# Kernel tuning notes

Hardware: AMD Instinct MI355X
Metric: run time of the kernel (lower is better)

## Reference

```python
import jax, jax.numpy as jnp
import numpy as np

B, C, H, W = 8, 64, 64, 64
OUT_H, OUT_W = 32, 32


def setup_inputs() -> dict:
    key = jax.random.key(0)
    ks = jax.random.split(key, 9)
    s = 1.0 / np.sqrt(C).astype(np.float32)
    return {
        "x": jax.random.normal(ks[0], (B, C, H, W), jnp.float32),
        "wq": jax.random.normal(ks[1], (C, C), jnp.float32) * s,
        "bq": jax.random.normal(ks[2], (C,), jnp.float32) * 0.01,
        "wk": jax.random.normal(ks[3], (C, C), jnp.float32) * s,
        "bk": jax.random.normal(ks[4], (C,), jnp.float32) * 0.01,
        "wv": jax.random.normal(ks[5], (C, C), jnp.float32) * s,
        "bv": jax.random.normal(ks[6], (C,), jnp.float32) * 0.01,
        "wm": jax.random.normal(ks[7], (C, C), jnp.float32) * s,
        "bm": jax.random.normal(ks[8], (C,), jnp.float32) * 0.01,
    }


def reference(x, wq, bq, wk, bk, wv, bv, wm, bm):
    # pushforward: self-attention over spatial tokens, 1x1-conv mixing + ReLU,
    # then bilinear resize to out_shape (align_corners=False semantics).
    b, c, h, w = x.shape
    t = x.reshape(b, c, h * w).transpose(0, 2, 1)  # [B, HW, C] tokens
    q = jnp.einsum('bnc,dc->bnd', t, wq) + bq      # 1x1 conv == per-pixel linear
    k = jnp.einsum('bnc,dc->bnd', t, wk) + bk
    v = jnp.einsum('bnc,dc->bnd', t, wv) + bv
    scores = jnp.einsum('bnc,bmc->bnm', q, k) / jnp.sqrt(jnp.float32(c))  # [B, HW, HW]
    attn = jax.nn.softmax(scores, axis=-1)
    o = jnp.einsum('bnm,bmc->bnc', attn, v)        # [B, HW, C]
    mixed = jax.nn.relu(jnp.einsum('bnc,dc->bnd', o, wm) + bm)
    out = mixed.transpose(0, 2, 1).reshape(b, c, h, w)
    # F.interpolate(mode='bilinear', align_corners=False) == half-pixel bilinear, no antialias
    out = jax.image.resize(out, (b, c, OUT_H, OUT_W), method='bilinear', antialias=False)
    return out
```

## Files before the change

### kernel.cpp

```cpp
#include <hip/hip_runtime.h>
#include <stdint.h>

typedef unsigned short u16;
typedef unsigned int   u32;
typedef __attribute__((ext_vector_type(8))) short short8;
typedef __attribute__((ext_vector_type(4))) float f32x4;

#define NTOK 4096
#define LOG2E 1.44269504088896340736f
#define QS    (0.125f * LOG2E)

__device__ __forceinline__ u16 f2bf(float f) {
    u32 u = __builtin_bit_cast(u32, f);
    u += 0x7fffu + ((u >> 16) & 1u);
    return (u16)(u >> 16);
}
__device__ __forceinline__ float bf2f(u16 v) {
    return __builtin_bit_cast(float, (u32)v << 16);
}
__device__ __forceinline__ u32 pk_hu(float a, float b) {
    u32 ua = __builtin_bit_cast(u32, a) + 0x8000u;
    u32 ub = __builtin_bit_cast(u32, b) + 0x8000u;
    return __builtin_amdgcn_perm(ub, ua, 0x07060302);
}

#define MFMA16x32 __builtin_amdgcn_mfma_f32_16x16x32_bf16

__global__ __launch_bounds__(256) void qkv_mfma4(
    const float* __restrict__ x,
    const float* __restrict__ wq, const float* __restrict__ bq,
    const float* __restrict__ wk, const float* __restrict__ bk,
    const float* __restrict__ wv, const float* __restrict__ bv,
    u16* __restrict__ Q, u16* __restrict__ K, u16* __restrict__ Vp)
{
    __shared__ __align__(16) u16 Wl[3 * 64 * 72];
    __shared__ __align__(16) u16 Xl[64 * 64];
    const int tid  = threadIdx.x;
    const int b    = blockIdx.x & 7;
    const int slab = blockIdx.x >> 3;
    const int n0   = slab << 6;
    const int wave = tid >> 6;
    const int lane = tid & 63;
    const int quad = lane >> 4;
    const int l15  = lane & 15;

#pragma unroll
    for (int j = 0; j < 12; ++j) {
        const float* src = (j < 4) ? wq : (j < 8) ? wk : wv;
        const float sc = (j < 4) ? QS : 1.0f;
        const int idx = (j & 3) * 1024 + tid * 4;
        const float4 v = *(const float4*)(src + idx);
        uint2 pk;
        pk.x = (u32)f2bf(v.x * sc) | ((u32)f2bf(v.y * sc) << 16);
        pk.y = (u32)f2bf(v.z * sc) | ((u32)f2bf(v.w * sc) << 16);
        *(uint2*)&Wl[(j >> 2) * 4608 + (idx >> 6) * 72 + (idx & 63)] = pk;
    }

    float4 xs[4];
#pragma unroll
    for (int g = 0; g < 4; ++g) {
        const int ch = g * 16 + wave * 4 + quad;
        xs[g] = *(const float4*)(x + ((size_t)(b * 64 + ch)) * NTOK + n0 + l15 * 4);
    }
#pragma unroll
    for (int g = 0; g < 4; ++g) {
        const int ch = g * 16 + wave * 4 + quad;
        const float vv[4] = {xs[g].x, xs[g].y, xs[g].z, xs[g].w};
#pragma unroll
        for (int e = 0; e < 4; ++e) {
            const int tok = l15 * 4 + e;
            Xl[tok * 64 + (((ch >> 3) ^ (tok & 7)) & 7) * 8 + (ch & 7)] = f2bf(vv[e]);
        }
    }
    __syncthreads();

    const int row0 = wave * 16 + l15;
    short8 xf[2];
#pragma unroll
    for (int kk = 0; kk < 2; ++kk)
        xf[kk] = *(const short8*)&Xl[row0 * 64 + (((kk * 4 + quad) ^ (row0 & 7)) & 7) * 8];

    const size_t tokbase = (size_t)b * NTOK + n0 + wave * 16;

#pragma unroll
    for (int mat = 0; mat < 2; ++mat) {
        const float* bias = (mat == 0) ? bq : bk;
        const float bsc = (mat == 0) ? QS : 1.0f;
#pragma unroll
        for (int mt = 0; mt < 4; ++mt) {
            const u16* wr = &Wl[mat * 4608 + (mt * 16 + l15) * 72 + quad * 8];
            const short8 wf0 = *(const short8*)(wr);
            const short8 wf1 = *(const short8*)(wr + 32);
            f32x4 acc = {0.f, 0.f, 0.f, 0.f};
            acc = MFMA16x32(wf0, xf[0], acc, 0, 0, 0);
            acc = MFMA16x32(wf1, xf[1], acc, 0, 0, 0);
            const float4 b4 = *(const float4*)(bias + mt * 16 + quad * 4);
            uint2 pk;
            pk.x = (u32)f2bf(acc[0] + b4.x * bsc) | ((u32)f2bf(acc[1] + b4.y * bsc) << 16);
            pk.y = (u32)f2bf(acc[2] + b4.z * bsc) | ((u32)f2bf(acc[3] + b4.w * bsc) << 16);
            u16* dst = (mat == 0) ? Q : K;
            *(uint2*)(dst + (tokbase + l15) * 64 + mt * 16 + quad * 4) = pk;
        }
    }

    __syncthreads();
    u16* Vl = Xl;
    const int tok = wave * 16 + l15;
#pragma unroll
    for (int mt = 0; mt < 4; ++mt) {
        const u16* wr = &Wl[2 * 4608 + (mt * 16 + l15) * 72 + quad * 8];
        const short8 wf0 = *(const short8*)(wr);
        const short8 wf1 = *(const short8*)(wr + 32);
        f32x4 acc = {0.f, 0.f, 0.f, 0.f};
        acc = MFMA16x32(wf0, xf[0], acc, 0, 0, 0);
        acc = MFMA16x32(wf1, xf[1], acc, 0, 0, 0);
        const float4 b4 = *(const float4*)(bv + mt * 16 + quad * 4);
        const float o[4] = {acc[0] + b4.x, acc[1] + b4.y, acc[2] + b4.z, acc[3] + b4.w};
#pragma unroll
        for (int r = 0; r < 4; ++r) {
            const int d = mt * 16 + quad * 4 + r;
            Vl[d * 64 + (((tok >> 3) ^ ((d >> 1) & 7)) & 7) * 8 + (tok & 7)] = f2bf(o[r]);
        }
    }
    __syncthreads();

#pragma unroll
    for (int dd = 0; dd < 4; ++dd) {
        const int d2   = (tid >> 4) + dd * 16;
        const int tok0 = (tid & 15) * 4;
        const int slot = ((tok0 >> 3) ^ ((d2 >> 1) & 7)) & 7;
        const uint2 v2 = *(const uint2*)&Vl[d2 * 64 + slot * 8 + (tok0 & 7)];
        const int gt = slab * 2 + (tok0 >> 5);
        *(uint2*)(Vp + (((size_t)b * 128 + gt) * 64 + d2) * 32 + (tok0 & 31)) = v2;
    }
}

__global__ __launch_bounds__(512, 2) void attn6(
    const u16* __restrict__ Q, const u16* __restrict__ K,
    const u16* __restrict__ Vp,
    const float* __restrict__ wm, const float* __restrict__ bm,
    float* __restrict__ out)
{
    __shared__ __align__(16) char smem[54272];
    const int tid  = threadIdx.x;
    const int wave = tid >> 6;
    const int lane = tid & 63;
    const int quad = lane >> 4;
    const int l15  = lane & 15;
    const int h    = wave >> 2;
    const int s    = wave & 3;
    const int b    = blockIdx.x & 7;
    const int oh   = blockIdx.x >> 3;
    const int n0   = oh * 128;

    const u16* qbase = Q + ((size_t)(b * NTOK + n0 + h * 64 + l15)) * 64 + quad * 8;
    short8 qf[4][2];
#pragma unroll
    for (int nt = 0; nt < 4; ++nt)
#pragma unroll
        for (int kk = 0; kk < 2; ++kk)
            qf[nt][kk] = *(const short8*)(qbase + nt * 1024 + kk * 32);

    const u16* Kb  = K + ((size_t)b * NTOK + s * 1024) * 64;
    const u16* Vbp = Vp + ((size_t)b * 128 + s * 32) * 2048;
    u16* Pw = (u16*)(smem + wave * 4096);

    short8 onesB;
#pragma unroll
    for (int j = 0; j < 8; ++j) onesB[j] = (short)0x3F80;

    f32x4 O[4][4];
#pragma unroll
    for (int nt = 0; nt < 4; ++nt)
#pragma unroll
        for (int ct = 0; ct < 4; ++ct) O[nt][ct] = (f32x4){0.f, 0.f, 0.f, 0.f};
    f32x4 lpa[4] = {{0.f,0.f,0.f,0.f},{0.f,0.f,0.f,0.f},{0.f,0.f,0.f,0.f},{0.f,0.f,0.f,0.f}};

    short8 kf[2][2], vf[4], kf_n[2][2], vf_n[4];
#pragma unroll
    for (int mtk = 0; mtk < 2; ++mtk)
#pragma unroll
        for (int kk = 0; kk < 2; ++kk)
            kf[mtk][kk] = *(const short8*)(Kb + (mtk * 16 + l15) * 64 + kk * 32 + quad * 8);
#pragma unroll
    for (int ct = 0; ct < 4; ++ct)
        vf[ct] = *(const short8*)(Vbp + (ct * 16 + l15) * 32 + quad * 8);

#pragma unroll 1
    for (int t = 0; t < 32; ++t) {
#pragma unroll
        for (int mtk = 0; mtk < 2; ++mtk) {
#pragma unroll
            for (int nt = 0; nt < 4; ++nt) {
                f32x4 sv = {0.f, 0.f, 0.f, 0.f};
                sv = MFMA16x32(kf[mtk][0], qf[nt][0], sv, 0, 0, 0);
                sv = MFMA16x32(kf[mtk][1], qf[nt][1], sv, 0, 0, 0);
                const float p0 = __builtin_amdgcn_exp2f(sv[0]);
                const float p1 = __builtin_amdgcn_exp2f(sv[1]);
                const float p2 = __builtin_amdgcn_exp2f(sv[2]);
                const float p3 = __builtin_amdgcn_exp2f(sv[3]);
                uint2 pk;
                pk.x = pk_hu(p0, p1);
                pk.y = pk_hu(p2, p3);
                const int wp = (mtk * 4 + quad) ^ (l15 & 6);
                *(uint2*)(Pw + (nt * 16 + l15) * 32 + wp * 4) = pk;
            }
        }
        if (t < 31) {
            const u16* kt = Kb + (size_t)(t + 1) * 2048;
#pragma unroll
            for (int mtk = 0; mtk < 2; ++mtk)
#pragma unroll
                for (int kk = 0; kk < 2; ++kk)
                    kf_n[mtk][kk] = *(const short8*)(kt + (mtk * 16 + l15) * 64 + kk * 32 + quad * 8);
        }
#pragma unroll
        for (int nt = 0; nt < 4; ++nt) {
            const int s16 = quad ^ ((l15 >> 1) & 3);
            const short8 pf = *(const short8*)(Pw + (nt * 16 + l15) * 32 + s16 * 8);
            lpa[nt] = MFMA16x32(pf, onesB, lpa[nt], 0, 0, 0);
#pragma unroll
            for (int ct = 0; ct < 4; ++ct)
                O[nt][ct] = MFMA16x32(pf, vf[ct], O[nt][ct], 0, 0, 0);
        }
        if (t < 31) {
#pragma unroll
            for (int ct = 0; ct < 4; ++ct)
                vf_n[ct] = *(const short8*)(Vbp + (size_t)(t + 1) * 2048 + (ct * 16 + l15) * 32 + quad * 8);
#pragma unroll
            for (int mtk = 0; mtk < 2; ++mtk)
#pragma unroll
                for (int kk = 0; kk < 2; ++kk) kf[mtk][kk] = kf_n[mtk][kk];
#pragma unroll
            for (int ct = 0; ct < 4; ++ct) vf[ct] = vf_n[ct];
        }
    }

    __syncthreads();

    if (l15 == 0) {
        float* lpw = (float*)(smem + 52224 + (h * 4 + s) * 256);
#pragma unroll
        for (int nt = 0; nt < 4; ++nt)
            *(f32x4*)(lpw + nt * 16 + quad * 4) = lpa[nt];
    }
    if (s != 0) {
        u16* sec = (u16*)smem + (h * 3 + s - 1) * 4352;
#pragma unroll
        for (int nt = 0; nt < 4; ++nt)
#pragma unroll
            for (int ct = 0; ct < 4; ++ct)
#pragma unroll
                for (int r = 0; r < 4; ++r)
                    sec[(nt * 16 + quad * 4 + r) * 68 + ct * 16 + l15] = f2bf(O[nt][ct][r]);
    }
    __syncthreads();

    float rinv[4][4];
    if (s == 0) {
#pragma unroll
        for (int nt = 0; nt < 4; ++nt)
#pragma unroll
            for (int r = 0; r < 4; ++r) {
                const int row = nt * 16 + quad * 4 + r;
                float sum = 0.f;
#pragma unroll
                for (int sx = 0; sx < 4; ++sx)
                    sum += ((const float*)(smem + 52224 + (h * 4 + sx) * 256))[row];
                rinv[nt][r] = 1.0f / sum;
            }
#pragma unroll
        for (int sx = 1; sx < 4; ++sx) {
            const u16* sec = (const u16*)smem + (h * 3 + sx - 1) * 4352;
#pragma unroll
            for (int nt = 0; nt < 4; ++nt)
#pragma unroll
                for (int ct = 0; ct < 4; ++ct)
#pragma unroll
                    for (int r = 0; r < 4; ++r)
                        O[nt][ct][r] += bf2f(sec[(nt * 16 + quad * 4 + r) * 68 + ct * 16 + l15]);
        }
    }
    short8 wB[4][2];
    float bb[4];
#pragma unroll
    for (int nt = 0; nt < 4; ++nt) {
        const int d = nt * 16 + l15;
        const float* wr = wm + (size_t)d * 64 + quad * 8;
        const float4 a0 = *(const float4*)(wr);
        const float4 a1 = *(const float4*)(wr + 4);
        const float4 c0 = *(const float4*)(wr + 32);
        const float4 c1 = *(const float4*)(wr + 36);
        ((u32*)&wB[nt][0])[0] = (u32)f2bf(a0.x) | ((u32)f2bf(a0.y) << 16);
        ((u32*)&wB[nt][0])[1] = (u32)f2bf(a0.z) | ((u32)f2bf(a0.w) << 16);
        ((u32*)&wB[nt][0])[2] = (u32)f2bf(a1.x) | ((u32)f2bf(a1.y) << 16);
        ((u32*)&wB[nt][0])[3] = (u32)f2bf(a1.z) | ((u32)f2bf(a1.w) << 16);
        ((u32*)&wB[nt][1])[0] = (u32)f2bf(c0.x) | ((u32)f2bf(c0.y) << 16);
        ((u32*)&wB[nt][1])[1] = (u32)f2bf(c0.z) | ((u32)f2bf(c0.w) << 16);
        ((u32*)&wB[nt][1])[2] = (u32)f2bf(c1.x) | ((u32)f2bf(c1.y) << 16);
        ((u32*)&wB[nt][1])[3] = (u32)f2bf(c1.z) | ((u32)f2bf(c1.w) << 16);
        bb[nt] = bm[d];
    }
    __syncthreads();

    if (s == 0) {
        u16* M0 = (u16*)smem + h * 4096;
#pragma unroll
        for (int nt = 0; nt < 4; ++nt)
#pragma unroll
            for (int ct = 0; ct < 4; ++ct)
#pragma unroll
                for (int r = 0; r < 4; ++r) {
                    const int lr = nt * 16 + quad * 4 + r;
                    const int ch = ct * 16 + l15;
                    const float v = O[nt][ct][r] * rinv[nt][r];
                    M0[lr * 64 + (((ch >> 3) ^ (lr & 7)) & 7) * 8 + (ch & 7)] = f2bf(v);
                }
    }
    __syncthreads();

    const u16* M0r = (const u16*)smem + (wave >> 2) * 4096;
    const int lr = (wave & 3) * 16 + l15;
    const short8 af0 = *(const short8*)&M0r[lr * 64 + ((quad ^ (lr & 7)) & 7) * 8];
    const short8 af1 = *(const short8*)&M0r[lr * 64 + (((4 + quad) ^ (lr & 7)) & 7) * 8];
    float* Mf = (float*)(smem + 16384);
#pragma unroll
    for (int nt = 0; nt < 4; ++nt) {
        f32x4 acc = {0.f, 0.f, 0.f, 0.f};
        acc = MFMA16x32(af0, wB[nt][0], acc, 0, 0, 0);
        acc = MFMA16x32(af1, wB[nt][1], acc, 0, 0, 0);
#pragma unroll
        for (int r = 0; r < 4; ++r) {
            float v = acc[r] + bb[nt];
            v = v > 0.f ? v : 0.f;
            Mf[(wave * 16 + quad * 4 + r) * 68 + nt * 16 + l15] = v;
        }
    }
    __syncthreads();

    const int ow = tid & 31;
    const int cb = (tid >> 5) & 15;
#pragma unroll
    for (int i = 0; i < 4; ++i) {
        const int c = cb + i * 16;
        const float v = 0.25f * (Mf[(2 * ow) * 68 + c] + Mf[(2 * ow + 1) * 68 + c]
                               + Mf[(64 + 2 * ow) * 68 + c] + Mf[(65 + 2 * ow) * 68 + c]);
        out[((size_t)(b * 64 + c) * 32 + oh) * 32 + ow] = v;
    }
}

extern "C" void kernel_launch(void* const* d_in, const int* in_sizes, int n_in,
                              void* d_out, int out_size, void* d_ws, size_t ws_size,
                              hipStream_t stream) {
    (void)in_sizes; (void)n_in; (void)out_size; (void)ws_size;
    const float* x  = (const float*)d_in[0];
    const float* wq = (const float*)d_in[1];
    const float* bq = (const float*)d_in[2];
    const float* wk = (const float*)d_in[3];
    const float* bk = (const float*)d_in[4];
    const float* wv = (const float*)d_in[5];
    const float* bv = (const float*)d_in[6];
    const float* wm = (const float*)d_in[7];
    const float* bm = (const float*)d_in[8];

    u16* Q  = (u16*)d_ws;
    u16* K  = Q + (size_t)8 * NTOK * 64;
    u16* Vp = K + (size_t)8 * NTOK * 64;

    qkv_mfma4<<<512, 256, 0, stream>>>(x, wq, bq, wk, bk, wv, bv, Q, K, Vp);
    attn6<<<256, 512, 0, stream>>>(Q, K, Vp, wm, bm, (float*)d_out);
}
```

Measured before the change: 136.7 us.

## Switch attention to 32x32x16 MFMA with register-resident P and double-buffered K/V

Rewrites the attention inner loop to use 32x32x16 bf16 MFMA tiles instead of 16x16x32. The probability tile is no longer sent through LDS: it is re-laid out in registers with a cross-half-wave shuffle and fed straight into the PV MFMA. Row sums are now plain VALU adds rather than an MFMA against a ones matrix. K/V fragments are double-buffered across an unrolled pair of tiles. The aim is to cut LDS traffic, extra MFMAs and waits, at the cost of larger accumulators and higher register pressure.

```diff
diff --git a/kernel.cpp b/kernel.cpp
--- a/kernel.cpp
+++ b/kernel.cpp
@@ -3,8 +3,9 @@
 
 typedef unsigned short u16;
 typedef unsigned int   u32;
-typedef __attribute__((ext_vector_type(8))) short short8;
-typedef __attribute__((ext_vector_type(4))) float f32x4;
+typedef __attribute__((ext_vector_type(8)))  short short8;
+typedef __attribute__((ext_vector_type(4)))  float f32x4;
+typedef __attribute__((ext_vector_type(16))) float f32x16;
 
 #define NTOK 4096
 #define LOG2E 1.44269504088896340736f
@@ -23,8 +24,15 @@
     u32 ub = __builtin_bit_cast(u32, b) + 0x8000u;
     return __builtin_amdgcn_perm(ub, ua, 0x07060302);
 }
+__device__ __forceinline__ f32x16 zero16() {
+    f32x16 v;
+#pragma unroll
+    for (int i = 0; i < 16; ++i) v[i] = 0.f;
+    return v;
+}
 
 #define MFMA16x32 __builtin_amdgcn_mfma_f32_16x16x32_bf16
+#define MFMA32x16 __builtin_amdgcn_mfma_f32_32x32x16_bf16
 
 __global__ __launch_bounds__(256) void qkv_mfma4(
     const float* __restrict__ x,
@@ -135,7 +143,7 @@
     }
 }
 
-__global__ __launch_bounds__(512, 2) void attn6(
+__global__ __launch_bounds__(512, 2) void attn7(
     const u16* __restrict__ Q, const u16* __restrict__ K,
     const u16* __restrict__ Vp,
     const float* __restrict__ wm, const float* __restrict__ bm,
@@ -145,6 +153,8 @@
     const int tid  = threadIdx.x;
     const int wave = tid >> 6;
     const int lane = tid & 63;
+    const int c31  = lane & 31;
+    const int hw   = lane >> 5;
     const int quad = lane >> 4;
     const int l15  = lane & 15;
     const int h    = wave >> 2;
@@ -153,132 +163,143 @@
     const int oh   = blockIdx.x >> 3;
     const int n0   = oh * 128;
 
-    const u16* qbase = Q + ((size_t)(b * NTOK + n0 + h * 64 + l15)) * 64 + quad * 8;
-    short8 qf[4][2];
-#pragma unroll
-    for (int nt = 0; nt < 4; ++nt)
-#pragma unroll
-        for (int kk = 0; kk < 2; ++kk)
-            qf[nt][kk] = *(const short8*)(qbase + nt * 1024 + kk * 32);
+    short8 qf[2][4];
+#pragma unroll
+    for (int nt = 0; nt < 2; ++nt)
+#pragma unroll
+        for (int ks = 0; ks < 4; ++ks)
+            qf[nt][ks] = *(const short8*)(Q + ((size_t)(b * NTOK + n0 + h * 64 + nt * 32 + c31)) * 64
+                                            + ks * 16 + hw * 8);
 
     const u16* Kb  = K + ((size_t)b * NTOK + s * 1024) * 64;
     const u16* Vbp = Vp + ((size_t)b * 128 + s * 32) * 2048;
-    u16* Pw = (u16*)(smem + wave * 4096);
-
-    short8 onesB;
-#pragma unroll
-    for (int j = 0; j < 8; ++j) onesB[j] = (short)0x3F80;
-
-    f32x4 O[4][4];
-#pragma unroll
-    for (int nt = 0; nt < 4; ++nt)
-#pragma unroll
-        for (int ct = 0; ct < 4; ++ct) O[nt][ct] = (f32x4){0.f, 0.f, 0.f, 0.f};
-    f32x4 lpa[4] = {{0.f,0.f,0.f,0.f},{0.f,0.f,0.f,0.f},{0.f,0.f,0.f,0.f},{0.f,0.f,0.f,0.f}};
-
-    short8 kf[2][2], vf[4], kf_n[2][2], vf_n[4];
-#pragma unroll
-    for (int mtk = 0; mtk < 2; ++mtk)
-#pragma unroll
-        for (int kk = 0; kk < 2; ++kk)
-            kf[mtk][kk] = *(const short8*)(Kb + (mtk * 16 + l15) * 64 + kk * 32 + quad * 8);
-#pragma unroll
-    for (int ct = 0; ct < 4; ++ct)
-        vf[ct] = *(const short8*)(Vbp + (ct * 16 + l15) * 32 + quad * 8);
+
+    f32x16 O[2][2];
+#pragma unroll
+    for (int mt = 0; mt < 2; ++mt)
+#pragma unroll
+        for (int nt = 0; nt < 2; ++nt) O[mt][nt] = zero16();
+    float lpa[2] = {0.f, 0.f};
+
+    auto load_kv = [&](short8 (&kf)[4], short8 (&vf)[4], int t) {
+        const int tc = (t < 32) ? t : 31;
+        const u16* kt = Kb + (size_t)tc * 2048;
+#pragma unroll
+        for (int ks = 0; ks < 4; ++ks)
+            kf[ks] = *(const short8*)(kt + c31 * 64 + ks * 16 + hw * 8);
+        const u16* vt = Vbp + (size_t)tc * 2048;
+#pragma unroll
+        for (int mk = 0; mk < 4; ++mk)
+            vf[mk] = *(const short8*)(vt + ((mk >> 1) * 32 + c31) * 32 + (mk & 1) * 16 + hw * 8);
+    };
+
+    auto tile_tail = [&](const f32x16 (&sv)[2], const short8 (&vf)[4]) {
+#pragma unroll
+        for (int nt = 0; nt < 2; ++nt) {
+            float p[16];
+#pragma unroll
+            for (int r = 0; r < 16; ++r) p[r] = __builtin_amdgcn_exp2f(sv[nt][r]);
+            lpa[nt] += (((p[0] + p[1]) + (p[2] + p[3])) + ((p[4] + p[5]) + (p[6] + p[7])))
+                     + (((p[8] + p[9]) + (p[10] + p[11])) + ((p[12] + p[13]) + (p[14] + p[15])));
+            u32 g[8];
+#pragma unroll
+            for (int gi = 0; gi < 8; ++gi) g[gi] = pk_hu(p[2 * gi], p[2 * gi + 1]);
+            const u32 rA = __shfl_xor(hw ? g[0] : g[2], 32);
+            const u32 rB = __shfl_xor(hw ? g[1] : g[3], 32);
+            const u32 rC = __shfl_xor(hw ? g[4] : g[6], 32);
+            const u32 rD = __shfl_xor(hw ? g[5] : g[7], 32);
+            uint4 B0, B1;
+            B0.x = hw ? rA : g[0];  B0.y = hw ? rB : g[1];
+            B0.z = hw ? g[2] : rA;  B0.w = hw ? g[3] : rB;
+            B1.x = hw ? rC : g[4];  B1.y = hw ? rD : g[5];
+            B1.z = hw ? g[6] : rC;  B1.w = hw ? g[7] : rD;
+            const short8 pb0 = __builtin_bit_cast(short8, B0);
+            const short8 pb1 = __builtin_bit_cast(short8, B1);
+            O[0][nt] = MFMA32x16(vf[0], pb0, O[0][nt], 0, 0, 0);
+            O[0][nt] = MFMA32x16(vf[1], pb1, O[0][nt], 0, 0, 0);
+            O[1][nt] = MFMA32x16(vf[2], pb0, O[1][nt], 0, 0, 0);
+            O[1][nt] = MFMA32x16(vf[3], pb1, O[1][nt], 0, 0, 0);
+        }
+    };
+
+    short8 kfA[4], vfA[4], kfB[4], vfB[4];
+    load_kv(kfA, vfA, 0);
 
 #pragma unroll 1
-    for (int t = 0; t < 32; ++t) {
-#pragma unroll
-        for (int mtk = 0; mtk < 2; ++mtk) {
-#pragma unroll
-            for (int nt = 0; nt < 4; ++nt) {
-                f32x4 sv = {0.f, 0.f, 0.f, 0.f};
-                sv = MFMA16x32(kf[mtk][0], qf[nt][0], sv, 0, 0, 0);
-                sv = MFMA16x32(kf[mtk][1], qf[nt][1], sv, 0, 0, 0);
-                const float p0 = __builtin_amdgcn_exp2f(sv[0]);
-                const float p1 = __builtin_amdgcn_exp2f(sv[1]);
-                const float p2 = __builtin_amdgcn_exp2f(sv[2]);
-                const float p3 = __builtin_amdgcn_exp2f(sv[3]);
-                uint2 pk;
-                pk.x = pk_hu(p0, p1);
-                pk.y = pk_hu(p2, p3);
-                const int wp = (mtk * 4 + quad) ^ (l15 & 6);
-                *(uint2*)(Pw + (nt * 16 + l15) * 32 + wp * 4) = pk;
-            }
-        }
-        if (t < 31) {
-            const u16* kt = Kb + (size_t)(t + 1) * 2048;
-#pragma unroll
-            for (int mtk = 0; mtk < 2; ++mtk)
-#pragma unroll
-                for (int kk = 0; kk < 2; ++kk)
-                    kf_n[mtk][kk] = *(const short8*)(kt + (mtk * 16 + l15) * 64 + kk * 32 + quad * 8);
-        }
-#pragma unroll
-        for (int nt = 0; nt < 4; ++nt) {
-            const int s16 = quad ^ ((l15 >> 1) & 3);
-            const short8 pf = *(const short8*)(Pw + (nt * 16 + l15) * 32 + s16 * 8);
-            lpa[nt] = MFMA16x32(pf, onesB, lpa[nt], 0, 0, 0);
-#pragma unroll
-            for (int ct = 0; ct < 4; ++ct)
-                O[nt][ct] = MFMA16x32(pf, vf[ct], O[nt][ct], 0, 0, 0);
-        }
-        if (t < 31) {
-#pragma unroll
-            for (int ct = 0; ct < 4; ++ct)
-                vf_n[ct] = *(const short8*)(Vbp + (size_t)(t + 1) * 2048 + (ct * 16 + l15) * 32 + quad * 8);
-#pragma unroll
-            for (int mtk = 0; mtk < 2; ++mtk)
-#pragma unroll
-                for (int kk = 0; kk < 2; ++kk) kf[mtk][kk] = kf_n[mtk][kk];
-#pragma unroll
-            for (int ct = 0; ct < 4; ++ct) vf[ct] = vf_n[ct];
-        }
-    }
-
-    __syncthreads();
-
-    if (l15 == 0) {
-        float* lpw = (float*)(smem + 52224 + (h * 4 + s) * 256);
-#pragma unroll
-        for (int nt = 0; nt < 4; ++nt)
-            *(f32x4*)(lpw + nt * 16 + quad * 4) = lpa[nt];
+    for (int tt = 0; tt < 16; ++tt) {
+        const int t0 = tt * 2;
+        f32x16 sv0[2];
+#pragma unroll
+        for (int nt = 0; nt < 2; ++nt) {
+            f32x16 a = zero16();
+            a = MFMA32x16(kfA[0], qf[nt][0], a, 0, 0, 0);
+            a = MFMA32x16(kfA[1], qf[nt][1], a, 0, 0, 0);
+            a = MFMA32x16(kfA[2], qf[nt][2], a, 0, 0, 0);
+            a = MFMA32x16(kfA[3], qf[nt][3], a, 0, 0, 0);
+            sv0[nt] = a;
+        }
+        load_kv(kfB, vfB, t0 + 1);
+        tile_tail(sv0, vfA);
+
+        f32x16 sv1[2];
+#pragma unroll
+        for (int nt = 0; nt < 2; ++nt) {
+            f32x16 a = zero16();
+            a = MFMA32x16(kfB[0], qf[nt][0], a, 0, 0, 0);
+            a = MFMA32x16(kfB[1], qf[nt][1], a, 0, 0, 0);
+            a = MFMA32x16(kfB[2], qf[nt][2], a, 0, 0, 0);
+            a = MFMA32x16(kfB[3], qf[nt][3], a, 0, 0, 0);
+            sv1[nt] = a;
+        }
+        load_kv(kfA, vfA, t0 + 2);
+        tile_tail(sv1, vfB);
+    }
+
+#pragma unroll
+    for (int nt = 0; nt < 2; ++nt) lpa[nt] += __shfl_xor(lpa[nt], 32);
+
+    float* lpbuf = (float*)(smem + 52224);
+    if (hw == 0) {
+#pragma unroll
+        for (int nt = 0; nt < 2; ++nt)
+            lpbuf[(h * 4 + s) * 64 + nt * 32 + c31] = lpa[nt];
     }
     if (s != 0) {
         u16* sec = (u16*)smem + (h * 3 + s - 1) * 4352;
 #pragma unroll
-        for (int nt = 0; nt < 4; ++nt)
-#pragma unroll
-            for (int ct = 0; ct < 4; ++ct)
-#pragma unroll
-                for (int r = 0; r < 4; ++r)
-                    sec[(nt * 16 + quad * 4 + r) * 68 + ct * 16 + l15] = f2bf(O[nt][ct][r]);
-    }
-    __syncthreads();
-
-    float rinv[4][4];
+        for (int mt = 0; mt < 2; ++mt)
+#pragma unroll
+            for (int nt = 0; nt < 2; ++nt)
+#pragma unroll
+                for (int r = 0; r < 16; ++r) {
+                    const int ch = mt * 32 + (r & 3) + 8 * (r >> 2) + 4 * hw;
+                    sec[(nt * 32 + c31) * 68 + ch] = f2bf(O[mt][nt][r]);
+                }
+    }
+    __syncthreads();
+
+    float rinv[2];
     if (s == 0) {
 #pragma unroll
-        for (int nt = 0; nt < 4; ++nt)
-#pragma unroll
-            for (int r = 0; r < 4; ++r) {
-                const int row = nt * 16 + quad * 4 + r;
-                float sum = 0.f;
-#pragma unroll
-                for (int sx = 0; sx < 4; ++sx)
-                    sum += ((const float*)(smem + 52224 + (h * 4 + sx) * 256))[row];
-                rinv[nt][r] = 1.0f / sum;
-            }
+        for (int nt = 0; nt < 2; ++nt) {
+            float sum = 0.f;
+#pragma unroll
+            for (int sx = 0; sx < 4; ++sx)
+                sum += lpbuf[(h * 4 + sx) * 64 + nt * 32 + c31];
+            rinv[nt] = 1.0f / sum;
+        }
 #pragma unroll
         for (int sx = 1; sx < 4; ++sx) {
             const u16* sec = (const u16*)smem + (h * 3 + sx - 1) * 4352;
 #pragma unroll
-            for (int nt = 0; nt < 4; ++nt)
-#pragma unroll
-                for (int ct = 0; ct < 4; ++ct)
-#pragma unroll
-                    for (int r = 0; r < 4; ++r)
-                        O[nt][ct][r] += bf2f(sec[(nt * 16 + quad * 4 + r) * 68 + ct * 16 + l15]);
+            for (int mt = 0; mt < 2; ++mt)
+#pragma unroll
+                for (int nt = 0; nt < 2; ++nt)
+#pragma unroll
+                    for (int r = 0; r < 16; ++r) {
+                        const int ch = mt * 32 + (r & 3) + 8 * (r >> 2) + 4 * hw;
+                        O[mt][nt][r] += bf2f(sec[(nt * 32 + c31) * 68 + ch]);
+                    }
         }
     }
     short8 wB[4][2];
@@ -291,7 +312,7 @@
         const float4 a1 = *(const float4*)(wr + 4);
         const float4 c0 = *(const float4*)(wr + 32);
         const float4 c1 = *(const float4*)(wr + 36);
-        ((u32*)&wB[nt][0])[0] = (u32)f2bf(a0.x) | ((u32)f2bf(a0.y) << 16);
+        ((u32*)&wB[nt][0])[0] = pk_hu(a0.y, a0.x) ^ 0u, ((u32*)&wB[nt][0])[0] = (u32)f2bf(a0.x) | ((u32)f2bf(a0.y) << 16);
         ((u32*)&wB[nt][0])[1] = (u32)f2bf(a0.z) | ((u32)f2bf(a0.w) << 16);
         ((u32*)&wB[nt][0])[2] = (u32)f2bf(a1.x) | ((u32)f2bf(a1.y) << 16);
         ((u32*)&wB[nt][0])[3] = (u32)f2bf(a1.z) | ((u32)f2bf(a1.w) << 16);
@@ -306,14 +327,14 @@
     if (s == 0) {
         u16* M0 = (u16*)smem + h * 4096;
 #pragma unroll
-        for (int nt = 0; nt < 4; ++nt)
-#pragma unroll
-            for (int ct = 0; ct < 4; ++ct)
-#pragma unroll
-                for (int r = 0; r < 4; ++r) {
-                    const int lr = nt * 16 + quad * 4 + r;
-                    const int ch = ct * 16 + l15;
-                    const float v = O[nt][ct][r] * rinv[nt][r];
+        for (int mt = 0; mt < 2; ++mt)
+#pragma unroll
+            for (int nt = 0; nt < 2; ++nt)
+#pragma unroll
+                for (int r = 0; r < 16; ++r) {
+                    const int lr = nt * 32 + c31;
+                    const int ch = mt * 32 + (r & 3) + 8 * (r >> 2) + 4 * hw;
+                    const float v = O[mt][nt][r] * rinv[nt];
                     M0[lr * 64 + (((ch >> 3) ^ (lr & 7)) & 7) * 8 + (ch & 7)] = f2bf(v);
                 }
     }
@@ -368,5 +389,5 @@
     u16* Vp = K + (size_t)8 * NTOK * 64;
 
     qkv_mfma4<<<512, 256, 0, stream>>>(x, wq, bq, wk, bk, wv, bv, Q, K, Vp);
-    attn6<<<256, 512, 0, stream>>>(Q, K, Vp, wm, bm, (float*)d_out);
-}
+    attn7<<<256, 512, 0, stream>>>(Q, K, Vp, wm, bm, (float*)d_out);
+}
```

After: 135.7 us. About the same (-0.8%).
